# Optimization experiments

Hardware: AMD Instinct MI355X
Metric: run time of the kernel (lower is better)

## Reference

```python
import jax, jax.numpy as jnp
import numpy as np

EMBED_DIM = 768
N_HEADS = 12
SEQ_LEN = 577
MAX_REL = 2


def _relative_position_indices(seq_len: int, max_rel: int) -> jnp.ndarray:
    """Static [S, S] int index map into the relative bias table."""
    n_patches = seq_len - 1
    n_per_dim = int(np.sqrt(n_patches))
    n_entries = (2 * max_rel - 1) ** 2
    cls_cls, cls_patch, patch_cls = n_entries, n_entries + 1, n_entries + 2
    idx = np.arange(seq_len)
    qy, qx = (idx - 1) // n_per_dim, (idx - 1) % n_per_dim
    ry = np.clip(qy[:, None] - qy[None, :], -max_rel + 1, max_rel - 1)
    rx = np.clip(qx[:, None] - qx[None, :], -max_rel + 1, max_rel - 1)
    patch_idx = (ry + max_rel - 1) * (2 * max_rel - 1) + (rx + max_rel - 1)
    is_cls = idx == 0
    out = np.where(is_cls[None, :], patch_cls, patch_idx)
    out = np.where(is_cls[:, None], cls_patch, out)
    out = np.where(is_cls[:, None] & is_cls[None, :], cls_cls, out)
    return jnp.asarray(out, dtype=jnp.int32)


def setup_inputs() -> dict:
    key = jax.random.key(0)
    ks = jax.random.split(key, 6)
    e = EMBED_DIM
    scale = 1.0 / np.sqrt(e)
    return {
        "x": jax.random.normal(ks[0], (32, SEQ_LEN, e), dtype=jnp.float32),
        "Wq": jax.random.normal(ks[1], (e, e), dtype=jnp.float32) * scale,
        "Wk": jax.random.normal(ks[2], (e, e), dtype=jnp.float32) * scale,
        "Wv": jax.random.normal(ks[3], (e, e), dtype=jnp.float32) * scale,
        "Wo": jax.random.normal(ks[4], (e, e), dtype=jnp.float32) * scale,
        "bo": jnp.zeros((e,), dtype=jnp.float32),
        "bias_table": jax.random.normal(ks[5], (12,), dtype=jnp.float32) * 0.02,
    }


def reference(x, Wq, Wk, Wv, Wo, bo, bias_table):
    b, s, e = x.shape
    h, d = N_HEADS, e // N_HEADS
    rel_idx = _relative_position_indices(s, MAX_REL)  # [S, S] int32 (static)

    q = (x @ Wq).reshape(b, s, h, d).transpose(0, 2, 1, 3)  # [b,h,s,d]
    k = (x @ Wk).reshape(b, s, h, d).transpose(0, 2, 1, 3)
    v = (x @ Wv).reshape(b, s, h, d).transpose(0, 2, 1, 3)

    scores = jnp.einsum('bhqd,bhkd->bhqk', q, k) / jnp.sqrt(jnp.float32(d))
    bias = jnp.take(bias_table, rel_idx, axis=0)  # [S, S]
    attn = jax.nn.softmax(scores + bias[None, None, :, :], axis=-1)

    out = jnp.einsum('bhqk,bhkd->bhqd', attn, v)
    out = out.transpose(0, 2, 1, 3).reshape(b, s, e)
    return out @ Wo + bo
```

## Files before the change

### kernel.cpp

```cpp
#include <hip/hip_runtime.h>

typedef unsigned short u16;
typedef short short8 __attribute__((ext_vector_type(8)));
typedef float floatx4 __attribute__((ext_vector_type(4)));

#define MFMA16(a, b, c) __builtin_amdgcn_mfma_f32_16x16x32_bf16((a), (b), (c), 0, 0, 0)

__device__ __forceinline__ u16 f2bf(float f) {
  unsigned u = __builtin_bit_cast(unsigned, f);
  u = (u + 0x7fffu + ((u >> 16) & 1u)) >> 16;
  return (u16)u;
}

__device__ __forceinline__ float bf2f(u16 u) {
  return __builtin_bit_cast(float, ((unsigned)u) << 16);
}

__device__ __forceinline__ float exp2hw(float x) {
  float r; asm("v_exp_f32 %0, %1" : "=v"(r) : "v"(x)); return r;
}

__device__ __forceinline__ unsigned cvtpk_bf16(float lo, float hi) {
  unsigned r;
  asm("v_cvt_pk_bf16_f32 %0, %1, %2" : "=v"(r) : "v"(lo), "v"(hi));
  return r;
}

__device__ __forceinline__ float bflo(unsigned u) {
  return __builtin_bit_cast(float, u << 16);
}
__device__ __forceinline__ float bfhi(unsigned u) {
  return __builtin_bit_cast(float, u & 0xffff0000u);
}

__device__ __forceinline__ void gload16(const void* g, void* l) {
  typedef __attribute__((address_space(1))) const void GV;
  typedef __attribute__((address_space(3))) void LV;
  __builtin_amdgcn_global_load_lds((GV*)g, (LV*)l, 16, 0, 0);
}


__global__ void cvt_x_kernel(const float* __restrict__ x, u16* __restrict__ xb, int n4) {
  int i = blockIdx.x * 256 + threadIdx.x;
  if (i >= n4) return;
  float4 v = ((const float4*)x)[i];
  ushort4 r; r.x = f2bf(v.x); r.y = f2bf(v.y); r.z = f2bf(v.z); r.w = f2bf(v.w);
  ((ushort4*)xb)[i] = r;
}

__global__ void cvt_wT_kernel(const float* __restrict__ in, u16* __restrict__ out) {
  __shared__ float tile[64][65];
  const int k0 = blockIdx.x * 64, n0 = blockIdx.y * 64;
  const int t = threadIdx.x;
  const int tr = t >> 6, tc = t & 63;
#pragma unroll
  for (int i = 0; i < 16; ++i) {
    int row = i * 4 + tr;
    tile[row][tc] = in[(size_t)(k0 + row) * 768 + n0 + tc];
  }
  __syncthreads();
#pragma unroll
  for (int i = 0; i < 16; ++i) {
    int row = i * 4 + tr;
    out[(size_t)(n0 + row) * 768 + k0 + tc] = f2bf(tile[tc][row]);
  }
}

__global__ void bias_kernel(const float* __restrict__ table, u16* __restrict__ bp) {
  int idx = blockIdx.x * 256 + threadIdx.x;
  if (idx >= 577 * 76) return;
  int q = idx / 76, kb = idx - q * 76;
  u16 o8[8];
#pragma unroll
  for (int j = 0; j < 8; ++j) {
    int k = kb * 8 + j;
    float v = 0.f;
    if (k <= 576) {
      int id;
      if (q == 0 && k == 0) id = 9;
      else if (q == 0) id = 10;
      else if (k == 0) id = 11;
      else {
        int qy = (q - 1) / 24, qx = (q - 1) % 24;
        int ky = (k - 1) / 24, kx = (k - 1) % 24;
        int ry = qy - ky; ry = ry < -1 ? -1 : (ry > 1 ? 1 : ry);
        int rx = qx - kx; rx = rx < -1 ? -1 : (rx > 1 ? 1 : rx);
        id = (ry + 1) * 3 + (rx + 1);
      }
      v = table[id] * 1.4426950408889634f;
    }
    o8[j] = f2bf(v);
  }
  *(uint4*)(bp + ((size_t)kb * 577 + q) * 8) = *(const uint4*)o8;
}

__global__ void bias576_kernel(const float* __restrict__ table, float* __restrict__ b576) {
  int q = blockIdx.x * 256 + threadIdx.x;
  if (q >= 577) return;
  int id;
  if (q == 0) id = 10;
  else {
    int qy = (q - 1) / 24, qx = (q - 1) % 24;
    int ry = qy - 23; ry = ry < -1 ? -1 : (ry > 1 ? 1 : ry);
    int rx = qx - 23; rx = rx < -1 ? -1 : (rx > 1 ? 1 : rx);
    id = (ry + 1) * 3 + (rx + 1);
  }
  b576[q] = table[id] * 1.4426950408889634f;
}


template <int MODE>
__global__ __launch_bounds__(512, 2) void gemm_kernel(
    const u16* __restrict__ A, const u16* __restrict__ BT,
    const int M, const int NBN,
    float* __restrict__ outF, const float* __restrict__ bvec,
    u16* __restrict__ qarr, u16* __restrict__ karr, u16* __restrict__ vTa) {
  constexpr int K = 768;
  __shared__ __align__(16) u16 smem[33792];
  u16* As = smem;
  u16* Bs = smem + 16384;
  u16* Cs = smem;

  const int nwg = gridDim.x;
  const int q8 = nwg >> 3, r8 = nwg & 7;
  const int xcd = blockIdx.x & 7, jj = blockIdx.x >> 3;
  const int bid = ((xcd < r8) ? xcd * (q8 + 1) : r8 * (q8 + 1) + (xcd - r8) * q8) + jj;

  const int nb = bid % NBN, mb = bid / NBN;
  const int tid = threadIdx.x;
  const int wid = tid >> 6, l = tid & 63;
  const int wrm = wid >> 2, wcn = wid & 3;
  const int l15 = l & 15, l4 = l >> 4;
  const int m0 = mb * 256, n0 = nb * 256;

  floatx4 acc[8][4];
#pragma unroll
  for (int i = 0; i < 8; ++i)
#pragma unroll
    for (int j = 0; j < 4; ++j) acc[i][j] = 0.f;

  const int r1 = tid >> 2;
  const int g1 = (tid & 3) * 8;

  auto stage = [&](int buf, int kt) {
    const int k0 = kt * 32 + g1;
    int ar0 = m0 + r1;       if (ar0 >= M) ar0 = M - 1;
    int ar1 = m0 + r1 + 128; if (ar1 >= M) ar1 = M - 1;
    gload16(A + (size_t)ar0 * K + k0, &As[buf * 8192 + tid * 8]);
    gload16(A + (size_t)ar1 * K + k0, &As[buf * 8192 + 4096 + tid * 8]);
    gload16(BT + (size_t)(n0 + r1) * K + k0, &Bs[buf * 8192 + tid * 8]);
    gload16(BT + (size_t)(n0 + r1 + 128) * K + k0, &Bs[buf * 8192 + 4096 + tid * 8]);
  };

  stage(0, 0);
  __syncthreads();
  int cur = 0;
  for (int kt = 0; kt < 24; ++kt) {
    if (kt + 1 < 24) stage(cur ^ 1, kt + 1);
    short8 af[8], bf[4];
#pragma unroll
    for (int mi = 0; mi < 8; ++mi)
      af[mi] = *(const short8*)&As[cur * 8192 + (wrm * 128 + mi * 16 + l15) * 32 + l4 * 8];
#pragma unroll
    for (int ni = 0; ni < 4; ++ni)
      bf[ni] = *(const short8*)&Bs[cur * 8192 + (wcn * 64 + ni * 16 + l15) * 32 + l4 * 8];
#pragma unroll
    for (int mi = 0; mi < 8; ++mi)
#pragma unroll
      for (int ni = 0; ni < 4; ++ni)
        acc[mi][ni] = MFMA16(af[mi], bf[ni], acc[mi][ni]);
    __syncthreads();
    cur ^= 1;
  }

  if constexpr (MODE == 0) {
    const int proj = nb / 3;
    const int h0 = (nb - proj * 3) * 4;
    const float qs = (proj == 0) ? 0.18033688011112042f : 1.0f;
#pragma unroll
    for (int p = 0; p < 2; ++p) {
      __syncthreads();
      if (wrm == p) {
#pragma unroll
        for (int mi = 0; mi < 8; ++mi)
#pragma unroll
          for (int i = 0; i < 4; ++i) {
            const int rloc = mi * 16 + l4 * 4 + i;
#pragma unroll
            for (int ni = 0; ni < 4; ++ni)
              Cs[rloc * 264 + wcn * 64 + ni * 16 + l15] = f2bf(acc[mi][ni][i] * qs);
          }
      }
      __syncthreads();
      const int r = tid & 127, ch = tid >> 7;
      const int mrow = m0 + p * 128 + r;
      if (mrow < M) {
        const int bq = mrow / 577, sq = mrow - bq * 577;
        const u16* src = Cs + r * 264 + ch * 64;
        if (proj < 2) {
          u16* dst = (proj == 0) ? qarr : karr;
          u16* base = dst + ((size_t)(bq * 12 + h0 + ch) * 577 + sq) * 64;
#pragma unroll
          for (int j2 = 0; j2 < 8; ++j2)
            *(uint4*)(base + j2 * 8) = *(const uint4*)(src + j2 * 8);
        } else {
          u16* vbase = vTa + ((size_t)(bq * 12 + h0 + ch) * 64) * 608 + sq;
#pragma unroll
          for (int dc = 0; dc < 8; ++dc) {
            const short8 vv = *(const short8*)(src + dc * 8);
#pragma unroll
            for (int jx = 0; jx < 8; ++jx)
              vbase[(size_t)(dc * 8 + jx) * 608] = (u16)vv[jx];
          }
        }
      }
    }
  } else {
#pragma unroll
    for (int mi = 0; mi < 8; ++mi) {
#pragma unroll
      for (int i = 0; i < 4; ++i) {
        const int mrow = m0 + wrm * 128 + mi * 16 + l4 * 4 + i;
        if (mrow >= M) continue;
#pragma unroll
        for (int ni = 0; ni < 4; ++ni) {
          const int ncol = n0 + wcn * 64 + ni * 16 + l15;
          outF[(size_t)mrow * 768 + ncol] = acc[mi][ni][i] + bvec[ncol];
        }
      }
    }
  }
}


__global__ __launch_bounds__(256, 2) void attn_kernel(
    const u16* __restrict__ qg, const u16* __restrict__ kg,
    const u16* __restrict__ vT, const u16* __restrict__ bp,
    const float* __restrict__ b576, u16* __restrict__ xa) {
  const int bid = (blockIdx.x & 7) * 240 + (blockIdx.x >> 3);
  const int bh = bid / 5, qblk = bid - bh * 5;
  const int tid = threadIdx.x;
  const int w = tid >> 6, l = tid & 63;
  const int l15 = l & 15, l4 = l >> 4;
  const int qbase = qblk * 128 + w * 32;

  const u16* qh = qg + (size_t)bh * 577 * 64;
  const u16* kh = kg + (size_t)bh * 577 * 64;
  const u16* vh = vT + (size_t)bh * 64 * 608;

  __shared__ u16 Ks[2][64 * 64];
  __shared__ u16 Vs[2][64 * 64];

  const int sr = tid >> 3;
  const int sb = tid & 7;
  const int ss = ((sr & 7) ^ ((2 * (sr >> 3)) & 7)) & 7;
  const int scol = (sb ^ ss) * 8;

  const int sig = ((l15 >> 2) << 3) + (l15 & 3);
  const int s0_ = ((l15 & 3) ^ ((2 * (l15 >> 2)) & 7)) & 7;
  const int s4_ = s0_ ^ 4;
  const int oK00 = sig * 64 + ((l4 ^ s0_) << 3);
  const int oK01 = sig * 64 + (((l4 + 4) ^ s0_) << 3);
  const int oK10 = (sig + 4) * 64 + ((l4 ^ s4_) << 3);
  const int oK11 = (sig + 4) * 64 + (((l4 + 4) ^ s4_) << 3);
  const int oK20 = oK00 + 32 * 64;
  const int oK21 = oK01 + 32 * 64;
  const int oK30 = oK10 + 32 * 64;
  const int oK31 = oK11 + 32 * 64;
  int oV[4][2];
#pragma unroll
  for (int df = 0; df < 4; ++df) {
    const int r = df * 16 + l15;
    const int sv = ((r & 7) ^ ((2 * (r >> 3)) & 7)) & 7;
    oV[df][0] = r * 64 + ((l4 ^ sv) << 3);
    oV[df][1] = r * 64 + (((l4 + 4) ^ sv) << 3);
  }

  short8 qf[2][2];
  int bq[2];
#pragma unroll
  for (int g = 0; g < 2; ++g) {
    int qr = qbase + g * 16 + l15; if (qr > 576) qr = 576;
    bq[g] = qr;
    qf[g][0] = *(const short8*)(qh + qr * 64 + l4 * 8);
    qf[g][1] = *(const short8*)(qh + qr * 64 + 32 + l4 * 8);
  }

  float m[2], lsum[2] = {1.f, 1.f};
  {
    const u16* kp = kh + 576 * 64 + l4 * 8;
    const short8 kA = *(const short8*)(kp);
    const short8 kB = *(const short8*)(kp + 32);
#pragma unroll
    for (int g = 0; g < 2; ++g) {
      float acc = 0.f;
#pragma unroll
      for (int j = 0; j < 8; ++j)
        acc += bf2f((u16)qf[g][0][j]) * bf2f((u16)kA[j]) +
               bf2f((u16)qf[g][1][j]) * bf2f((u16)kB[j]);
      acc += __shfl_xor(acc, 16);
      acc += __shfl_xor(acc, 32);
      m[g] = acc + b576[bq[g]];
    }
  }
  floatx4 o[2][4];
#pragma unroll
  for (int df = 0; df < 4; ++df)
#pragma unroll
    for (int i = 0; i < 4; ++i) {
      const float v5 = bf2f(vh[(size_t)(df * 16 + l4 * 4 + i) * 608 + 576]);
      o[0][df][i] = v5; o[1][df][i] = v5;
    }

  gload16(kh + (size_t)sr * 64 + scol, &Ks[0][sr * 64 + sb * 8]);
  gload16(kh + (size_t)(sr + 32) * 64 + scol, &Ks[0][(sr + 32) * 64 + sb * 8]);
  gload16(vh + (size_t)sr * 608 + scol, &Vs[0][sr * 64 + sb * 8]);
  gload16(vh + (size_t)(sr + 32) * 608 + scol, &Vs[0][(sr + 32) * 64 + sb * 8]);
  uint4 bcA0 = *(const uint4*)(bp + ((size_t)l4 * 577 + bq[0]) * 8);
  uint4 bcB0 = *(const uint4*)(bp + ((size_t)(l4 + 4) * 577 + bq[0]) * 8);
  uint4 bcA1 = *(const uint4*)(bp + ((size_t)l4 * 577 + bq[1]) * 8);
  uint4 bcB1 = *(const uint4*)(bp + ((size_t)(l4 + 4) * 577 + bq[1]) * 8);
  __syncthreads();

  for (int t = 0; t < 9; ++t) {
    const int cur = t & 1;
    uint4 nA0 = bcA0, nB0 = bcB0, nA1 = bcA1, nB1 = bcB1;
    if (t < 8) {
      const int nk = (t + 1) * 64;
      gload16(kh + (size_t)(nk + sr) * 64 + scol, &Ks[cur ^ 1][sr * 64 + sb * 8]);
      gload16(kh + (size_t)(nk + sr + 32) * 64 + scol, &Ks[cur ^ 1][(sr + 32) * 64 + sb * 8]);
      gload16(vh + (size_t)sr * 608 + nk + scol, &Vs[cur ^ 1][sr * 64 + sb * 8]);
      gload16(vh + (size_t)(sr + 32) * 608 + nk + scol, &Vs[cur ^ 1][(sr + 32) * 64 + sb * 8]);
      const int kba = (t + 1) * 8 + l4;
      nA0 = *(const uint4*)(bp + ((size_t)kba * 577 + bq[0]) * 8);
      nB0 = *(const uint4*)(bp + ((size_t)(kba + 4) * 577 + bq[0]) * 8);
      nA1 = *(const uint4*)(bp + ((size_t)kba * 577 + bq[1]) * 8);
      nB1 = *(const uint4*)(bp + ((size_t)(kba + 4) * 577 + bq[1]) * 8);
    }

    const u16* kb_ = &Ks[cur][0];
    const short8 K00 = *(const short8*)(kb_ + oK00);
    const short8 K01 = *(const short8*)(kb_ + oK01);
    const short8 K10 = *(const short8*)(kb_ + oK10);
    const short8 K11 = *(const short8*)(kb_ + oK11);
    const short8 K20 = *(const short8*)(kb_ + oK20);
    const short8 K21 = *(const short8*)(kb_ + oK21);
    const short8 K30 = *(const short8*)(kb_ + oK30);
    const short8 K31 = *(const short8*)(kb_ + oK31);

    floatx4 sA0[2], sA1[2], sB0[2], sB1[2];
    __builtin_amdgcn_s_setprio(1);
#pragma unroll
    for (int g = 0; g < 2; ++g) {
      floatx4 a0 = 0.f, a1 = 0.f, b0 = 0.f, b1 = 0.f;
      a0 = MFMA16(K00, qf[g][0], a0); a0 = MFMA16(K01, qf[g][1], a0);
      a1 = MFMA16(K10, qf[g][0], a1); a1 = MFMA16(K11, qf[g][1], a1);
      b0 = MFMA16(K20, qf[g][0], b0); b0 = MFMA16(K21, qf[g][1], b0);
      b1 = MFMA16(K30, qf[g][0], b1); b1 = MFMA16(K31, qf[g][1], b1);
      sA0[g] = a0; sA1[g] = a1; sB0[g] = b0; sB1[g] = b1;
    }
    __builtin_amdgcn_s_setprio(0);

    float v_[2][16];
#pragma unroll
    for (int g = 0; g < 2; ++g) {
      const uint4 ba = (g == 0) ? bcA0 : bcA1;
      const uint4 bb = (g == 0) ? bcB0 : bcB1;
      v_[g][0] = sA0[g][0] + bflo(ba.x);  v_[g][1] = sA0[g][1] + bfhi(ba.x);
      v_[g][2] = sA0[g][2] + bflo(ba.y);  v_[g][3] = sA0[g][3] + bfhi(ba.y);
      v_[g][4] = sA1[g][0] + bflo(ba.z);  v_[g][5] = sA1[g][1] + bfhi(ba.z);
      v_[g][6] = sA1[g][2] + bflo(ba.w);  v_[g][7] = sA1[g][3] + bfhi(ba.w);
      v_[g][8]  = sB0[g][0] + bflo(bb.x); v_[g][9]  = sB0[g][1] + bfhi(bb.x);
      v_[g][10] = sB0[g][2] + bflo(bb.y); v_[g][11] = sB0[g][3] + bfhi(bb.y);
      v_[g][12] = sB1[g][0] + bflo(bb.z); v_[g][13] = sB1[g][1] + bfhi(bb.z);
      v_[g][14] = sB1[g][2] + bflo(bb.w); v_[g][15] = sB1[g][3] + bfhi(bb.w);
    }

    float vm[2];
#pragma unroll
    for (int g = 0; g < 2; ++g) {
      float m0_ = fmaxf(v_[g][0], v_[g][1]),  m1_ = fmaxf(v_[g][2], v_[g][3]);
      float m2_ = fmaxf(v_[g][4], v_[g][5]),  m3_ = fmaxf(v_[g][6], v_[g][7]);
      float m4_ = fmaxf(v_[g][8], v_[g][9]),  m5_ = fmaxf(v_[g][10], v_[g][11]);
      float m6_ = fmaxf(v_[g][12], v_[g][13]), m7_ = fmaxf(v_[g][14], v_[g][15]);
      float a = fmaxf(fmaxf(m0_, m1_), fmaxf(m2_, m3_));
      float b = fmaxf(fmaxf(m4_, m5_), fmaxf(m6_, m7_));
      a = fmaxf(a, b);
      a = fmaxf(a, __shfl_xor(a, 16));
      a = fmaxf(a, __shfl_xor(a, 32));
      vm[g] = a;
    }

    if (__any((vm[0] > m[0] + 8.f) || (vm[1] > m[1] + 8.f))) {
      const float mn0 = fmaxf(m[0], vm[0]), mn1 = fmaxf(m[1], vm[1]);
      const float sc0 = exp2hw(m[0] - mn0), sc1 = exp2hw(m[1] - mn1);
      lsum[0] *= sc0; lsum[1] *= sc1;
#pragma unroll
      for (int df = 0; df < 4; ++df) { o[0][df] *= sc0; o[1][df] *= sc1; }
      m[0] = mn0; m[1] = mn1;
    }

    union PU { unsigned u[4]; short8 s; };
    PU pA[2], pB[2];
#pragma unroll
    for (int g = 0; g < 2; ++g) {
#pragma unroll
      for (int j = 0; j < 16; ++j) v_[g][j] = exp2hw(v_[g][j] - m[g]);
      float s0 = (v_[g][0] + v_[g][1]) + (v_[g][2] + v_[g][3]);
      float s1 = (v_[g][4] + v_[g][5]) + (v_[g][6] + v_[g][7]);
      float s2 = (v_[g][8] + v_[g][9]) + (v_[g][10] + v_[g][11]);
      float s3 = (v_[g][12] + v_[g][13]) + (v_[g][14] + v_[g][15]);
      float rs = (s0 + s1) + (s2 + s3);
      rs += __shfl_xor(rs, 16);
      rs += __shfl_xor(rs, 32);
      lsum[g] += rs;
#pragma unroll
      for (int j = 0; j < 4; ++j) {
        pA[g].u[j] = cvtpk_bf16(v_[g][2 * j], v_[g][2 * j + 1]);
        pB[g].u[j] = cvtpk_bf16(v_[g][8 + 2 * j], v_[g][8 + 2 * j + 1]);
      }
    }

    const u16* vb_ = &Vs[cur][0];
    const short8 vA0 = *(const short8*)(vb_ + oV[0][0]);
    const short8 vB0 = *(const short8*)(vb_ + oV[0][1]);
    const short8 vA1 = *(const short8*)(vb_ + oV[1][0]);
    const short8 vB1 = *(const short8*)(vb_ + oV[1][1]);
    const short8 vA2 = *(const short8*)(vb_ + oV[2][0]);
    const short8 vB2 = *(const short8*)(vb_ + oV[2][1]);
    const short8 vA3 = *(const short8*)(vb_ + oV[3][0]);
    const short8 vB3 = *(const short8*)(vb_ + oV[3][1]);

    __builtin_amdgcn_s_setprio(1);
#pragma unroll
    for (int g = 0; g < 2; ++g) {
      o[g][0] = MFMA16(vA0, pA[g].s, o[g][0]); o[g][0] = MFMA16(vB0, pB[g].s, o[g][0]);
      o[g][1] = MFMA16(vA1, pA[g].s, o[g][1]); o[g][1] = MFMA16(vB1, pB[g].s, o[g][1]);
      o[g][2] = MFMA16(vA2, pA[g].s, o[g][2]); o[g][2] = MFMA16(vB2, pB[g].s, o[g][2]);
      o[g][3] = MFMA16(vA3, pA[g].s, o[g][3]); o[g][3] = MFMA16(vB3, pB[g].s, o[g][3]);
    }
    __builtin_amdgcn_s_setprio(0);

    bcA0 = nA0; bcB0 = nB0; bcA1 = nA1; bcB1 = nB1;
    __syncthreads();
  }

  const int b = bh / 12, h = bh - (bh / 12) * 12;
#pragma unroll
  for (int g = 0; g < 2; ++g) {
    const int gq = qbase + g * 16 + l15;
    if (gq < 577) {
      const float inv = 1.f / lsum[g];
      u16* op = xa + ((size_t)(b * 577 + gq)) * 768 + h * 64 + l4 * 4;
#pragma unroll
      for (int d = 0; d < 4; ++d) {
        unsigned w0 = cvtpk_bf16(o[g][d][0] * inv, o[g][d][1] * inv);
        unsigned w1 = cvtpk_bf16(o[g][d][2] * inv, o[g][d][3] * inv);
        *(unsigned*)(op + d * 16) = w0;
        *(unsigned*)(op + d * 16 + 2) = w1;
      }
    }
  }
}


extern "C" void kernel_launch(void* const* d_in, const int* in_sizes, int n_in,
                              void* d_out, int out_size, void* d_ws, size_t ws_size,
                              hipStream_t stream) {
  const float* x  = (const float*)d_in[0];
  const float* Wq = (const float*)d_in[1];
  const float* Wk = (const float*)d_in[2];
  const float* Wv = (const float*)d_in[3];
  const float* Wo = (const float*)d_in[4];
  const float* bo = (const float*)d_in[5];
  const float* bt = (const float*)d_in[6];
  float* out = (float*)d_out;

  char* ws = (char*)d_ws;
  size_t off = 0;
  auto alloc = [&](size_t bytes) {
    void* p = ws + off;
    off += (bytes + 255) & ~(size_t)255;
    return p;
  };
  u16* xb   = (u16*)alloc((size_t)18464 * 768 * 2);
  u16* WT   = (u16*)alloc((size_t)2304 * 768 * 2);
  u16* WoT  = (u16*)alloc((size_t)768 * 768 * 2);
  u16* qa   = (u16*)alloc((size_t)384 * 577 * 64 * 2);
  u16* ka   = (u16*)alloc((size_t)384 * 577 * 64 * 2);
  u16* vT   = (u16*)alloc((size_t)384 * 64 * 608 * 2);
  u16* biasPk = (u16*)alloc((size_t)76 * 577 * 8 * 2);
  float* b576 = (float*)alloc((size_t)577 * 4);
  (void)ws_size; (void)in_sizes; (void)n_in; (void)out_size;

  cvt_x_kernel<<<(18464 * 768 / 4 + 255) / 256, 256, 0, stream>>>(x, xb, 18464 * 768 / 4);
  dim3 tg(12, 12);
  cvt_wT_kernel<<<tg, 256, 0, stream>>>(Wq, WT);
  cvt_wT_kernel<<<tg, 256, 0, stream>>>(Wk, WT + (size_t)768 * 768);
  cvt_wT_kernel<<<tg, 256, 0, stream>>>(Wv, WT + (size_t)2 * 768 * 768);
  cvt_wT_kernel<<<tg, 256, 0, stream>>>(Wo, WoT);
  bias_kernel<<<(577 * 76 + 255) / 256, 256, 0, stream>>>(bt, biasPk);
  bias576_kernel<<<3, 256, 0, stream>>>(bt, b576);

  gemm_kernel<0><<<73 * 9, 512, 0, stream>>>(xb, WT, 18464, 9,
                                             nullptr, nullptr, qa, ka, vT);
  attn_kernel<<<1920, 256, 0, stream>>>(qa, ka, vT, biasPk, b576, xb);
  gemm_kernel<1><<<73 * 3, 512, 0, stream>>>(xb, WoT, 18464, 3,
                                             out, bo, nullptr, nullptr, nullptr);
}
```

Before: 233.2 us.

## Deepen GEMM global-to-LDS pipeline to four stages with explicit vmcnt waits

Replaces the double-buffered GEMM K-loop with a four-slot LDS ring buffer that keeps three K-tiles of loads in flight. Each iteration waits with explicit s_waitcnt vmcnt counts and uses a single barrier instead of the trailing __syncthreads. Row pointers are hoisted out of the stage lambda, and MFMA issue is wrapped in s_setprio. The aim is to hide global load latency better. The cost is LDS growing from about 66KB to 128KB per block, which likely stops two 512-thread blocks from fitting on one CU despite the launch bounds.

Result: no change. 237.5 us (+1.8%).

```diff
diff --git a/kernel.cpp b/kernel.cpp
--- a/kernel.cpp
+++ b/kernel.cpp
@@ -116,9 +116,8 @@
     float* __restrict__ outF, const float* __restrict__ bvec,
     u16* __restrict__ qarr, u16* __restrict__ karr, u16* __restrict__ vTa) {
   constexpr int K = 768;
-  __shared__ __align__(16) u16 smem[33792];
-  u16* As = smem;
-  u16* Bs = smem + 16384;
+  constexpr int NKT = 24;
+  __shared__ __align__(16) u16 smem[4 * 16384];
   u16* Cs = smem;
 
   const int nwg = gridDim.x;
@@ -141,36 +140,51 @@
 
   const int r1 = tid >> 2;
   const int g1 = (tid & 3) * 8;
-
-  auto stage = [&](int buf, int kt) {
-    const int k0 = kt * 32 + g1;
-    int ar0 = m0 + r1;       if (ar0 >= M) ar0 = M - 1;
-    int ar1 = m0 + r1 + 128; if (ar1 >= M) ar1 = M - 1;
-    gload16(A + (size_t)ar0 * K + k0, &As[buf * 8192 + tid * 8]);
-    gload16(A + (size_t)ar1 * K + k0, &As[buf * 8192 + 4096 + tid * 8]);
-    gload16(BT + (size_t)(n0 + r1) * K + k0, &Bs[buf * 8192 + tid * 8]);
-    gload16(BT + (size_t)(n0 + r1 + 128) * K + k0, &Bs[buf * 8192 + 4096 + tid * 8]);
+  int ar0 = m0 + r1;       if (ar0 >= M) ar0 = M - 1;
+  int ar1 = m0 + r1 + 128; if (ar1 >= M) ar1 = M - 1;
+  const u16* pa0 = A + (size_t)ar0 * K + g1;
+  const u16* pa1 = A + (size_t)ar1 * K + g1;
+  const u16* pb0 = BT + (size_t)(n0 + r1) * K + g1;
+  const u16* pb1 = BT + (size_t)(n0 + r1 + 128) * K + g1;
+
+  auto stage = [&](int t) {
+    const int s = t & 3;
+    const int k0 = t * 32;
+    u16* base = &smem[s * 16384];
+    gload16(pa0 + k0, base + tid * 8);
+    gload16(pa1 + k0, base + 4096 + tid * 8);
+    gload16(pb0 + k0, base + 8192 + tid * 8);
+    gload16(pb1 + k0, base + 12288 + tid * 8);
   };
 
-  stage(0, 0);
-  __syncthreads();
-  int cur = 0;
-  for (int kt = 0; kt < 24; ++kt) {
-    if (kt + 1 < 24) stage(cur ^ 1, kt + 1);
+  stage(0); stage(1); stage(2);
+
+#pragma unroll 1
+  for (int t = 0; t < NKT; ++t) {
+    if (t <= 21)      asm volatile("s_waitcnt vmcnt(8)" ::: "memory");
+    else if (t == 22) asm volatile("s_waitcnt vmcnt(4)" ::: "memory");
+    else              asm volatile("s_waitcnt vmcnt(0)" ::: "memory");
+    __builtin_amdgcn_s_barrier();
+
+    if (t < NKT - 3) stage(t + 3);
+
+    const u16* sa = &smem[(t & 3) * 16384];
+    const u16* sbb = sa + 8192;
     short8 af[8], bf[4];
 #pragma unroll
     for (int mi = 0; mi < 8; ++mi)
-      af[mi] = *(const short8*)&As[cur * 8192 + (wrm * 128 + mi * 16 + l15) * 32 + l4 * 8];
+      af[mi] = *(const short8*)&sa[(wrm * 128 + mi * 16 + l15) * 32 + l4 * 8];
 #pragma unroll
     for (int ni = 0; ni < 4; ++ni)
-      bf[ni] = *(const short8*)&Bs[cur * 8192 + (wcn * 64 + ni * 16 + l15) * 32 + l4 * 8];
+      bf[ni] = *(const short8*)&sbb[(wcn * 64 + ni * 16 + l15) * 32 + l4 * 8];
+
+    __builtin_amdgcn_s_setprio(1);
 #pragma unroll
     for (int mi = 0; mi < 8; ++mi)
 #pragma unroll
       for (int ni = 0; ni < 4; ++ni)
         acc[mi][ni] = MFMA16(af[mi], bf[ni], acc[mi][ni]);
-    __syncthreads();
-    cur ^= 1;
+    __builtin_amdgcn_s_setprio(0);
   }
 
   if constexpr (MODE == 0) {
```
